# Kernel tuning notes

Measured on AMD Instinct MI355X. Metric: run time of the kernel, lower is better.

The kernel has to match this reference:

```python
import math
import jax, jax.numpy as jnp
import numpy as np

B, C, N, G = 8, 128, 1024, 8
CG = C // G  # channels per group = 16
EPS = 1e-5


def setup_inputs() -> dict:
    key = jax.random.key(0)
    k1, k2, k3 = jax.random.split(key, 3)
    points = jax.random.normal(k1, (B, C, N), dtype=jnp.float32)
    # grouped 1x1 Conv1d weight [C_out, C_in/groups, 1], bias [C]
    w = jax.random.normal(k2, (C, CG, 1), dtype=jnp.float32) * (1.0 / math.sqrt(CG))
    b = jax.random.normal(k3, (C,), dtype=jnp.float32) * 0.01
    gamma = jnp.ones((C,), dtype=jnp.float32)
    beta = jnp.zeros((C,), dtype=jnp.float32)
    return {"points": points, "w": w, "b": b, "gamma": gamma, "beta": beta}


def reference(points, w, b, gamma, beta):
    Bsz, Ch, Np = points.shape
    cg = Ch // G
    # grouped 1x1 conv: [B,G,Cg,N] x [G,Cg_out,Cg_in]
    x = points.reshape(Bsz, G, cg, Np)
    Wg = w.reshape(G, cg, cg)  # [group, out, in]
    t = jnp.einsum('goi,bgin->bgon', Wg, x) + b.reshape(1, G, cg, 1)  # [B,G,Cg,N]
    # attention: q=[B,G,N,Cg], k=[B,G,Cg,N] -> scores [B,G,N,N]
    scores = jnp.einsum('bgnc,bgcm->bgnm', t.transpose(0, 1, 3, 2), t) / math.sqrt(cg)
    att = jax.nn.softmax(scores, axis=-2)  # softmax over first N dim (dim=-2)
    v = jax.nn.elu(t)  # [B,G,Cg,N]
    out = jnp.einsum('bgcn,bgnm->bgcm', v, att)  # [B,G,Cg,N]
    # channel shuffle: transpose(1,2) then flatten -> [B,C,N]
    out = out.transpose(0, 2, 1, 3).reshape(Bsz, Ch, Np)
    out = out + points  # residual
    # GroupNorm(G, C)
    g = out.reshape(Bsz, G, cg, Np)
    mean = g.mean(axis=(2, 3), keepdims=True)
    var = ((g - mean) ** 2).mean(axis=(2, 3), keepdims=True)
    norm = ((g - mean) * jax.lax.rsqrt(var + EPS)).reshape(Bsz, Ch, Np)
    return norm * gamma[None, :, None] + beta[None, :, None]
```

## Files before the change

kernel.cpp:

```cpp
#include <hip/hip_runtime.h>
#include <hip/hip_fp16.h>

#define NB 8
#define NC 128
#define NN 1024
#define NG 8
#define NCG 16
#define GEPS 1e-5f
#define TPAD 20
#define VROW 1032

typedef _Float16 half4v __attribute__((ext_vector_type(4)));
typedef short short4v __attribute__((ext_vector_type(4)));
typedef float float4v __attribute__((ext_vector_type(4)));
typedef unsigned int uint2v __attribute__((ext_vector_type(2)));

__global__ __launch_bounds__(256)
void gsa_attn(const float* __restrict__ points, const float* __restrict__ w,
              const float* __restrict__ bias, float* __restrict__ y,
              float* __restrict__ stats)
{
    __shared__ __align__(16) _Float16 t_lds[NN][TPAD];
    __shared__ __align__(16) unsigned short v_lds[NCG][VROW];

    const int tid = threadIdx.x;
    const int bid = blockIdx.x;
    const int ms  = bid & 7;
    const int g   = (bid >> 3) & 7;
    const int b   = bid >> 6;

    const float* xg = points + ((size_t)(b * NC) + g * NCG) * NN;
    const float* wg = w + g * NCG * NCG;

    #pragma unroll
    for (int k = 0; k < 4; ++k) {
        const int n = (k << 8) + tid;
        float x[NCG];
        #pragma unroll
        for (int i = 0; i < NCG; ++i) x[i] = xg[(size_t)i * NN + n];
        _Float16 trow[NCG];
        #pragma unroll
        for (int o = 0; o < NCG; ++o) {
            float acc = bias[g * NCG + o];
            #pragma unroll
            for (int i = 0; i < NCG; ++i) acc = fmaf(wg[o * NCG + i], x[i], acc);
            trow[o] = (_Float16)(acc * 0.5f);
            const float ve = acc > 0.f ? acc : (__expf(acc) - 1.f);
            const unsigned int u = __builtin_bit_cast(unsigned int, ve);
            v_lds[o][n] = (unsigned short)((u + 0x8000u) >> 16);
        }
        #pragma unroll
        for (int q = 0; q < 4; ++q)
            *(half4v*)&t_lds[n][q * 4] = *(const half4v*)&trow[q * 4];
    }
    __syncthreads();

    const int lane = tid & 63;
    const int wv   = tid >> 6;
    const int lq   = lane & 15;
    const int lh   = lane >> 4;
    const int mw   = (ms << 7) + (wv << 5);

    const half4v bfrag0 = *(const half4v*)&t_lds[mw + lq][lh * 4];
    const half4v bfrag1 = *(const half4v*)&t_lds[mw + 16 + lq][lh * 4];

    float4v acc0 = {0.f, 0.f, 0.f, 0.f}, acc1 = {0.f, 0.f, 0.f, 0.f};
    float ssum0 = 0.f, ssum1 = 0.f;
    const float4v zz = {0.f, 0.f, 0.f, 0.f};

    #pragma unroll 4
    for (int nt = 0; nt < NN; nt += 16) {
        const half4v afrag = *(const half4v*)&t_lds[nt + lq][lh * 4];
        const short4v vfrag = *(const short4v*)&v_lds[lq][nt + lh * 4];

        float4v s0 = __builtin_amdgcn_mfma_f32_16x16x16f16(afrag, bfrag0, zz, 0, 0, 0);
        float4v s1 = __builtin_amdgcn_mfma_f32_16x16x16f16(afrag, bfrag1, zz, 0, 0, 0);

        float p0[4], p1[4];
        #pragma unroll
        for (int r = 0; r < 4; ++r) { p0[r] = __expf(s0[r]); p1[r] = __expf(s1[r]); }
        ssum0 += (p0[0] + p0[1]) + (p0[2] + p0[3]);
        ssum1 += (p1[0] + p1[1]) + (p1[2] + p1[3]);

        unsigned int pk00, pk01, pk10, pk11;
        asm("v_cvt_pk_bf16_f32 %0, %1, %2" : "=v"(pk00) : "v"(p0[0]), "v"(p0[1]));
        asm("v_cvt_pk_bf16_f32 %0, %1, %2" : "=v"(pk01) : "v"(p0[2]), "v"(p0[3]));
        asm("v_cvt_pk_bf16_f32 %0, %1, %2" : "=v"(pk10) : "v"(p1[0]), "v"(p1[1]));
        asm("v_cvt_pk_bf16_f32 %0, %1, %2" : "=v"(pk11) : "v"(p1[2]), "v"(p1[3]));
        uint2v u0; u0[0] = pk00; u0[1] = pk01;
        uint2v u1; u1[0] = pk10; u1[1] = pk11;

        acc0 = __builtin_amdgcn_mfma_f32_16x16x16bf16_1k(vfrag, __builtin_bit_cast(short4v, u0), acc0, 0, 0, 0);
        acc1 = __builtin_amdgcn_mfma_f32_16x16x16bf16_1k(vfrag, __builtin_bit_cast(short4v, u1), acc1, 0, 0, 0);
    }

    ssum0 += __shfl_xor(ssum0, 16); ssum0 += __shfl_xor(ssum0, 32);
    ssum1 += __shfl_xor(ssum1, 16); ssum1 += __shfl_xor(ssum1, 32);
    const float rs0 = 1.0f / ssum0, rs1 = 1.0f / ssum1;

    float gs[2] = {0.f, 0.f}, gq[2] = {0.f, 0.f};
    #pragma unroll
    for (int mt = 0; mt < 2; ++mt) {
        const float rs = mt ? rs1 : rs0;
        const int m = mw + mt * 16 + lq;
        #pragma unroll
        for (int r = 0; r < 4; ++r) {
            const int c = lh * 4 + r;
            const size_t oi = ((size_t)(b * NC) + (c * NG + g)) * NN + m;
            const float a = mt ? acc1[r] : acc0[r];
            const float val = fmaf(a, rs, points[oi]);
            y[oi] = val;
            gs[r >> 1] += val;
            gq[r >> 1] += val * val;
        }
    }
    #pragma unroll
    for (int j = 0; j < 2; ++j) {
        float a = gs[j], q = gq[j];
        #pragma unroll
        for (int off = 1; off <= 8; off <<= 1) {
            a += __shfl_xor(a, off);
            q += __shfl_xor(q, off);
        }
        if (lq == 0) {
            atomicAdd(&stats[(b * NG + lh * 2 + j) * 2 + 0], a);
            atomicAdd(&stats[(b * NG + lh * 2 + j) * 2 + 1], q);
        }
    }
}

__global__ __launch_bounds__(256)
void gsa_norm(const float* __restrict__ stats, const float* __restrict__ gamma,
              const float* __restrict__ beta, float* __restrict__ y)
{
    const int idx = blockIdx.x * 256 + threadIdx.x;
    const size_t base = (size_t)idx * 4;
    const int c = (int)((base >> 10) & (NC - 1));
    const int b = (int)(base >> 17);
    const int gp = c >> 4;

    const float s0 = stats[(b * NG + gp) * 2 + 0];
    const float s1 = stats[(b * NG + gp) * 2 + 1];
    const float inv = 1.0f / (float)(NCG * NN);
    const float mean = s0 * inv;
    const float var = fmaxf(s1 * inv - mean * mean, 0.f);
    const float sc = rsqrtf(var + GEPS) * gamma[c];
    const float sh = fmaf(-mean, sc, beta[c]);

    float4 v = *reinterpret_cast<const float4*>(y + base);
    v.x = fmaf(v.x, sc, sh);
    v.y = fmaf(v.y, sc, sh);
    v.z = fmaf(v.z, sc, sh);
    v.w = fmaf(v.w, sc, sh);
    *reinterpret_cast<float4*>(y + base) = v;
}

extern "C" void kernel_launch(void* const* d_in, const int* in_sizes, int n_in,
                              void* d_out, int out_size, void* d_ws, size_t ws_size,
                              hipStream_t stream)
{
    const float* points = (const float*)d_in[0];
    const float* w      = (const float*)d_in[1];
    const float* bias   = (const float*)d_in[2];
    const float* gamma  = (const float*)d_in[3];
    const float* beta   = (const float*)d_in[4];
    float* y     = (float*)d_out;
    float* stats = (float*)d_ws;

    hipMemsetAsync(stats, 0, NB * NG * 2 * sizeof(float), stream);
    gsa_attn<<<NB * NG * 8, 256, 0, stream>>>(points, w, bias, y, stats);
    gsa_norm<<<NB * NC * NN / 4 / 256, 256, 0, stream>>>(stats, gamma, beta, y);
}
```

Baseline: 120.3 us.

## Split grouped conv into separate kernel writing t and v to global workspace

The grouped 1x1 conv and ELU move out of the attention kernel into their own kernel. It writes fp16 t and bf16 v to a global workspace once, instead of each of the 8 m-slice blocks recomputing the whole group's conv into LDS. The attention kernel now reads its fragments straight from global memory (through the cache) with no LDS and no block barrier. This removes 8x redundant conv work and the LDS footprint, which may raise occupancy. The cost is an extra kernel launch, a global round trip for t and v, and uncoalesced per-lane global fragment loads in the inner loop.

```diff
diff --git a/kernel.cpp b/kernel.cpp
--- a/kernel.cpp
+++ b/kernel.cpp
@@ -7,53 +7,69 @@
 #define NG 8
 #define NCG 16
 #define GEPS 1e-5f
-#define TPAD 20
-#define VROW 1032
 
 typedef _Float16 half4v __attribute__((ext_vector_type(4)));
+typedef _Float16 half8v __attribute__((ext_vector_type(8)));
 typedef short short4v __attribute__((ext_vector_type(4)));
 typedef float float4v __attribute__((ext_vector_type(4)));
 typedef unsigned int uint2v __attribute__((ext_vector_type(2)));
 
+#define WS_STATS 0
+#define WS_T     4096
+#define WS_V     (4096 + 2097152)
+
 __global__ __launch_bounds__(256)
-void gsa_attn(const float* __restrict__ points, const float* __restrict__ w,
-              const float* __restrict__ bias, float* __restrict__ y,
+void gsa_conv(const float* __restrict__ points, const float* __restrict__ w,
+              const float* __restrict__ bias, _Float16* __restrict__ t_glob,
+              unsigned short* __restrict__ v_glob)
+{
+    const int tid  = threadIdx.x;
+    const int bid  = blockIdx.x;
+    const int pair = bid >> 2;
+    const int n    = ((bid & 3) << 8) + tid;
+    const int g    = pair & 7;
+
+    const float* xg = points + (size_t)pair * NCG * NN;
+    const float* wg = w + g * NCG * NCG;
+
+    float x[NCG];
+    #pragma unroll
+    for (int i = 0; i < NCG; ++i) x[i] = xg[(size_t)i * NN + n];
+
+    _Float16 trow[NCG];
+    float ve[NCG];
+    #pragma unroll
+    for (int o = 0; o < NCG; ++o) {
+        float acc = bias[g * NCG + o];
+        #pragma unroll
+        for (int i = 0; i < NCG; ++i) acc = fmaf(wg[o * NCG + i], x[i], acc);
+        trow[o] = (_Float16)(acc * 0.5f);
+        ve[o] = acc > 0.f ? acc : (__expf(acc) - 1.f);
+    }
+
+    _Float16* tp = t_glob + ((size_t)pair * NN + n) * NCG;
+    *(half8v*)(tp)     = *(const half8v*)&trow[0];
+    *(half8v*)(tp + 8) = *(const half8v*)&trow[8];
+
+    unsigned short* vp = v_glob + (size_t)pair * NCG * NN + n;
+    #pragma unroll
+    for (int o = 0; o < NCG; ++o) {
+        const unsigned int u = __builtin_bit_cast(unsigned int, ve[o]);
+        vp[(size_t)o * NN] = (unsigned short)((u + 0x8000u) >> 16);
+    }
+}
+
+__global__ __launch_bounds__(256)
+void gsa_attn(const float* __restrict__ points, const _Float16* __restrict__ t_glob,
+              const unsigned short* __restrict__ v_glob, float* __restrict__ y,
               float* __restrict__ stats)
 {
-    __shared__ __align__(16) _Float16 t_lds[NN][TPAD];
-    __shared__ __align__(16) unsigned short v_lds[NCG][VROW];
-
-    const int tid = threadIdx.x;
-    const int bid = blockIdx.x;
-    const int ms  = bid & 7;
-    const int g   = (bid >> 3) & 7;
-    const int b   = bid >> 6;
-
-    const float* xg = points + ((size_t)(b * NC) + g * NCG) * NN;
-    const float* wg = w + g * NCG * NCG;
-
-    #pragma unroll
-    for (int k = 0; k < 4; ++k) {
-        const int n = (k << 8) + tid;
-        float x[NCG];
-        #pragma unroll
-        for (int i = 0; i < NCG; ++i) x[i] = xg[(size_t)i * NN + n];
-        _Float16 trow[NCG];
-        #pragma unroll
-        for (int o = 0; o < NCG; ++o) {
-            float acc = bias[g * NCG + o];
-            #pragma unroll
-            for (int i = 0; i < NCG; ++i) acc = fmaf(wg[o * NCG + i], x[i], acc);
-            trow[o] = (_Float16)(acc * 0.5f);
-            const float ve = acc > 0.f ? acc : (__expf(acc) - 1.f);
-            const unsigned int u = __builtin_bit_cast(unsigned int, ve);
-            v_lds[o][n] = (unsigned short)((u + 0x8000u) >> 16);
-        }
-        #pragma unroll
-        for (int q = 0; q < 4; ++q)
-            *(half4v*)&t_lds[n][q * 4] = *(const half4v*)&trow[q * 4];
-    }
-    __syncthreads();
+    const int tid  = threadIdx.x;
+    const int bid  = blockIdx.x;
+    const int ms   = bid & 7;
+    const int pair = bid >> 3;
+    const int g    = pair & 7;
+    const int b    = pair >> 3;
 
     const int lane = tid & 63;
     const int wv   = tid >> 6;
@@ -61,17 +77,23 @@
     const int lh   = lane >> 4;
     const int mw   = (ms << 7) + (wv << 5);
 
-    const half4v bfrag0 = *(const half4v*)&t_lds[mw + lq][lh * 4];
-    const half4v bfrag1 = *(const half4v*)&t_lds[mw + 16 + lq][lh * 4];
+    const _Float16* tp = t_glob + (size_t)pair * NN * NCG;
+    const unsigned short* vp = v_glob + (size_t)pair * NCG * NN;
+
+    const half4v bfrag0 = *(const half4v*)(tp + (size_t)(mw + lq) * NCG + lh * 4);
+    const half4v bfrag1 = *(const half4v*)(tp + (size_t)(mw + 16 + lq) * NCG + lh * 4);
 
     float4v acc0 = {0.f, 0.f, 0.f, 0.f}, acc1 = {0.f, 0.f, 0.f, 0.f};
     float ssum0 = 0.f, ssum1 = 0.f;
     const float4v zz = {0.f, 0.f, 0.f, 0.f};
 
+    const _Float16* ap = tp + (size_t)lq * NCG + lh * 4;
+    const unsigned short* vvp = vp + (size_t)lq * NN + lh * 4;
+
     #pragma unroll 4
     for (int nt = 0; nt < NN; nt += 16) {
-        const half4v afrag = *(const half4v*)&t_lds[nt + lq][lh * 4];
-        const short4v vfrag = *(const short4v*)&v_lds[lq][nt + lh * 4];
+        const half4v afrag  = *(const half4v*)(ap + (size_t)nt * NCG);
+        const short4v vfrag = *(const short4v*)(vvp + nt);
 
         float4v s0 = __builtin_amdgcn_mfma_f32_16x16x16f16(afrag, bfrag0, zz, 0, 0, 0);
         float4v s1 = __builtin_amdgcn_mfma_f32_16x16x16f16(afrag, bfrag1, zz, 0, 0, 0);
@@ -164,10 +186,15 @@
     const float* bias   = (const float*)d_in[2];
     const float* gamma  = (const float*)d_in[3];
     const float* beta   = (const float*)d_in[4];
-    float* y     = (float*)d_out;
-    float* stats = (float*)d_ws;
+    float* y = (float*)d_out;
+
+    char* ws = (char*)d_ws;
+    float* stats = (float*)(ws + WS_STATS);
+    _Float16* t_glob = (_Float16*)(ws + WS_T);
+    unsigned short* v_glob = (unsigned short*)(ws + WS_V);
 
     hipMemsetAsync(stats, 0, NB * NG * 2 * sizeof(float), stream);
-    gsa_attn<<<NB * NG * 8, 256, 0, stream>>>(points, w, bias, y, stats);
+    gsa_conv<<<NB * NG * 4, 256, 0, stream>>>(points, w, bias, t_glob, v_glob);
+    gsa_attn<<<NB * NG * 8, 256, 0, stream>>>(points, t_glob, v_glob, y, stats);
     gsa_norm<<<NB * NC * NN / 4 / 256, 256, 0, stream>>>(stats, gamma, beta, y);
 }
```

New measurement: 117.3 us. -2.5%, faster.
